# Optimization experiments

Hardware: AMD Instinct MI355X
Metric: run time of the kernel (lower is better)

The kernel has to match this reference:

```python
import jax, jax.numpy as jnp
import numpy as np

B, T, F = 1024, 256, 64
H1, H2, H3 = 64, 32, 16


def _lstm_params(key, in_dim, units, scale=0.1):
    k1, k2, k3 = jax.random.split(key, 3)
    W = jax.random.normal(k1, (in_dim, 4 * units), jnp.float32) * scale
    U = jax.random.normal(k2, (units, 4 * units), jnp.float32) * scale
    b = jax.random.normal(k3, (4 * units,), jnp.float32) * scale
    return W, U, b


def lstm_seq(x, W, U, b, reverse):
    """Keras-style LSTM (gate order i,f,g,o). Returns (all_h [B,T,H] time-aligned, last_h [B,H])."""
    Bx = x.shape[0]
    H = U.shape[0]
    xz = jnp.einsum('bti,ij->btj', x, W) + b  # [B,T,4H]
    if reverse:
        xz = xz[:, ::-1]
    xz = jnp.swapaxes(xz, 0, 1)  # [T,B,4H]

    def step(carry, zx):
        h, c = carry
        z = zx + h @ U
        i, f, g, o = jnp.split(z, 4, axis=-1)
        i = jax.nn.sigmoid(i)
        f = jax.nn.sigmoid(f)
        g = jnp.tanh(g)
        o = jax.nn.sigmoid(o)
        c = f * c + i * g
        h = o * jnp.tanh(c)
        return (h, c), h

    h0 = jnp.zeros((Bx, H), x.dtype)
    (hT, _), hs = jax.lax.scan(step, (h0, h0), xz)
    hs = jnp.swapaxes(hs, 0, 1)  # [B,T,H]
    if reverse:
        hs = hs[:, ::-1]  # Keras Bidirectional re-reverses backward outputs
    return hs, hT


def setup_inputs() -> dict:
    key = jax.random.key(0)
    ks = jax.random.split(key, 10)
    x = jax.random.normal(ks[0], (B, T, F), jnp.float32)
    W1f, U1f, b1f = _lstm_params(ks[1], F, H1)
    W1b, U1b, b1b = _lstm_params(ks[2], F, H1)
    W2f, U2f, b2f = _lstm_params(ks[3], 2 * H1, H2)
    W2b, U2b, b2b = _lstm_params(ks[4], 2 * H1, H2)
    W3f, U3f, b3f = _lstm_params(ks[5], 2 * H2, H3)
    W3b, U3b, b3b = _lstm_params(ks[6], 2 * H2, H3)
    Wd1 = jax.random.normal(ks[7], (2 * H3, 16), jnp.float32) * 0.1
    bd1 = jnp.zeros((16,), jnp.float32)
    Wd2 = jax.random.normal(ks[8], (16, 2), jnp.float32) * 0.1
    bd2 = jnp.zeros((2,), jnp.float32)
    return dict(inputs=x,
                W1f=W1f, U1f=U1f, b1f=b1f, W1b=W1b, U1b=U1b, b1b=b1b,
                W2f=W2f, U2f=U2f, b2f=b2f, W2b=W2b, U2b=U2b, b2b=b2b,
                W3f=W3f, U3f=U3f, b3f=b3f, W3b=W3b, U3b=U3b, b3b=b3b,
                Wd1=Wd1, bd1=bd1, Wd2=Wd2, bd2=bd2)


def reference(inputs,
              W1f, U1f, b1f, W1b, U1b, b1b,
              W2f, U2f, b2f, W2b, U2b, b2b,
              W3f, U3f, b3f, W3b, U3b, b3b,
              Wd1, bd1, Wd2, bd2):
    # inference path: all dropout / GaussianDropout layers are identity
    hf, _ = lstm_seq(inputs, W1f, U1f, b1f, reverse=False)
    hb, _ = lstm_seq(inputs, W1b, U1b, b1b, reverse=True)
    x = jnp.concatenate([hf, hb], axis=-1)  # [B,T,128]

    hf, _ = lstm_seq(x, W2f, U2f, b2f, reverse=False)
    hb, _ = lstm_seq(x, W2b, U2b, b2b, reverse=True)
    x = jnp.concatenate([hf, hb], axis=-1)  # [B,T,64]

    _, hf_last = lstm_seq(x, W3f, U3f, b3f, reverse=False)
    _, hb_last = lstm_seq(x, W3b, U3b, b3b, reverse=True)
    x = jnp.concatenate([hf_last, hb_last], axis=-1)  # [B,32] (Flatten is identity)

    x = jnp.clip(x @ Wd1 + bd1, 0.0, 6.0)  # relu6
    logits = x @ Wd2 + bd2
    return jax.nn.softmax(logits, axis=-1)
```

## Files before the change

kernel.cpp:

```cpp
#include <hip/hip_runtime.h>
#include <hip/hip_bf16.h>

#define T_SEQ 256
#define BATCH 1024

typedef __attribute__((ext_vector_type(8))) short  short8;
typedef __attribute__((ext_vector_type(4))) short  short4v;
typedef __attribute__((ext_vector_type(4))) float  floatx4;
typedef unsigned short ushort_t;
typedef unsigned int   uint_t;

template <int P> struct IC { static constexpr int v = P; };

constexpr float NL2E = -1.4426950408889634f;
constexpr float L2E2 =  2.8853900817779268f;

__device__ __forceinline__ float exp2_fast(float x) {
    float r; asm("v_exp_f32 %0, %1" : "=v"(r) : "v"(x)); return r;
}
__device__ __forceinline__ float rcp_fast(float x) {
    float r; asm("v_rcp_f32 %0, %1" : "=v"(r) : "v"(x)); return r;
}
__device__ __forceinline__ ushort_t f2bf(float f) {
    union { float f; uint_t u; } v; v.f = f;
    uint_t r = v.u + 0x7FFFu + ((v.u >> 16) & 1u);
    return (ushort_t)(r >> 16);
}
__device__ __forceinline__ uint_t pk_bf16(float a, float b) {
    union { __hip_bfloat162 h; uint_t u; } v;
    v.h = __float22bfloat162_rn(make_float2(a, b));
    return v.u;
}
__device__ __forceinline__ void sync_lds() {
    asm volatile("s_waitcnt lgkmcnt(0)\n\ts_barrier" ::: "memory");
}

__device__ __forceinline__ floatx4 mfma16(short4v a, short4v b, floatx4 c) {
#if __has_builtin(__builtin_amdgcn_mfma_f32_16x16x16bf16_1k)
    return __builtin_amdgcn_mfma_f32_16x16x16bf16_1k(a, b, c, 0, 0, 0);
#else
    floatx4 d;
    asm("v_mfma_f32_16x16x16_bf16 %0, %1, %2, %3" : "=v"(d) : "v"(a), "v"(b), "v"(c));
    return d;
#endif
}

template <int D, int H, bool IS_FIRST, bool SEQ_OUT, int MODE>
__global__ __launch_bounds__(MODE == 2 ? 64 : 64 * (H / 16), 1) void lstm_fused(
    const void* __restrict__ xin,
    const float* __restrict__ Wf, const float* __restrict__ Uf, const float* __restrict__ bgf,
    const float* __restrict__ Wb, const float* __restrict__ Ub, const float* __restrict__ bgb,
    void* __restrict__ outp)
{
    constexpr bool SW   = (MODE >= 1);
    constexpr bool REGH = (MODE == 2);
    constexpr int UG  = REGH ? 1 : H / 16;
    constexpr int NT  = REGH ? H / 16 : 1;
    constexpr int KSx = D / 32;
    constexpr int KSh = REGH ? 1 : (H + 31) / 32;
    constexpr int NC  = REGH ? H / 16 : 1;
    constexpr int HP  = (H < 32 ? 32 : H) + 8;
    constexpr int G4  = 4 * H;
    constexpr int NTH = 64 * UG;
    static_assert(D % 32 == 0 && T_SEQ % 4 == 0, "shape");

    const int tid  = threadIdx.x;
    const int ug   = tid >> 6;
    const int lane = tid & 63;
    const int lm   = lane & 15;
    const int lq   = lane >> 4;
    const int dir  = blockIdx.y;
    const int b0   = blockIdx.x * 16;

    const float* W  = dir ? Wb  : Wf;
    const float* U  = dir ? Ub  : Uf;
    const float* bg = dir ? bgb : bgf;

    __shared__ __align__(16) ushort_t hbuf[REGH ? 8 : 2 * 16 * HP];

    short8  aw[4][NT][KSx];
    short8  hw[4][NT][KSh];
    short4v uw[4][NT][NC];
    floatx4 bias4[4][NT];
#pragma unroll
    for (int g = 0; g < 4; g++) {
        const float sc = (g == 2) ? L2E2 : NL2E;
#pragma unroll
        for (int t = 0; t < NT; t++) {
            const int ub = g * H + (REGH ? t * 16 : ug * 16);
            floatx4 b4;
#pragma unroll
            for (int r = 0; r < 4; r++)
                b4[r] = sc * bg[ub + (SW ? lq * 4 + r : lm)];
            bias4[g][t] = b4;
            const int nc = ub + lm;
#pragma unroll
            for (int ks = 0; ks < KSx; ks++) {
                short8 f;
#pragma unroll
                for (int e = 0; e < 8; e++)
                    f[e] = (short)f2bf(sc * W[(ks * 32 + lq * 8 + e) * G4 + nc]);
                aw[g][t][ks] = f;
            }
            if constexpr (!REGH) {
#pragma unroll
                for (int ks = 0; ks < KSh; ks++) {
                    short8 f;
#pragma unroll
                    for (int e = 0; e < 8; e++) {
                        const int k = ks * 32 + lq * 8 + e;
                        f[e] = (k < H) ? (short)f2bf(sc * U[k * G4 + nc]) : (short)0;
                    }
                    hw[g][t][ks] = f;
                }
            } else {
#pragma unroll
                for (int c = 0; c < NC; c++) {
                    short4v f;
#pragma unroll
                    for (int e = 0; e < 4; e++)
                        f[e] = (short)f2bf(sc * U[(c * 16 + lq * 4 + e) * G4 + nc]);
                    uw[g][t][c] = f;
                }
            }
        }
    }

    if constexpr (!REGH) {
        for (int idx = tid; idx < 2 * 16 * HP; idx += NTH)
            hbuf[idx] = 0;
    }

    float   cst[NT][4];
    float   hl[NT][4];
    short4v hfrag[NC];
#pragma unroll
    for (int t = 0; t < NT; t++)
#pragma unroll
        for (int r = 0; r < 4; r++) { cst[t][r] = 0.f; hl[t][r] = 0.f; }
    if constexpr (REGH) {
#pragma unroll
        for (int c = 0; c < NC; c++) hfrag[c] = (short4v){0, 0, 0, 0};
    }

    const int t0 = dir ? T_SEQ - 1 : 0;
    const float*    pxf = (const float*)xin + ((size_t)(b0 + lm) * T_SEQ + t0) * D + lq * 8;
    const ushort_t* pxb = (const ushort_t*)xin + ((size_t)t0 * BATCH + b0 + lm) * D + lq * 8;
    const long xstepf = dir ? -(long)D : (long)D;
    const long xstepb = (dir ? -(long)BATCH : (long)BATCH) * D;
    ushort_t* pout;
    if constexpr (SW)
        pout = (ushort_t*)outp + ((size_t)t0 * BATCH + b0 + lm) * (2 * H) + dir * H +
               (REGH ? 0 : ug * 16) + lq * 4;
    else
        pout = (ushort_t*)outp + ((size_t)t0 * BATCH + b0 + lq * 4) * (2 * H) + dir * H +
               ug * 16 + lm;
    const long ostep = (dir ? -(long)BATCH : (long)BATCH) * (2 * H);

    float4 rawf[4][2 * KSx];
    short8 rawb[4][KSx];

    auto load_slot = [&](auto sl_) {
        constexpr int SL = decltype(sl_)::v;
        if (IS_FIRST) {
#pragma unroll
            for (int ks = 0; ks < KSx; ks++) {
                rawf[SL][2 * ks + 0] = *(const float4*)(pxf + ks * 32 + 0);
                rawf[SL][2 * ks + 1] = *(const float4*)(pxf + ks * 32 + 4);
            }
            pxf += xstepf;
        } else {
#pragma unroll
            for (int ks = 0; ks < KSx; ks++)
                rawb[SL][ks] = *(const short8*)(pxb + ks * 32);
            pxb += xstepb;
        }
    };

    load_slot(IC<0>{}); load_slot(IC<1>{}); load_slot(IC<2>{}); load_slot(IC<3>{});
    if constexpr (!REGH) __syncthreads();

    auto step = [&](auto p_, auto sl_, int s) {
        constexpr int P  = decltype(p_)::v;
        constexpr int SL = decltype(sl_)::v;

        short8 fh[KSh];
        if constexpr (!REGH) {
#pragma unroll
            for (int ks = 0; ks < KSh; ks++)
                fh[ks] = *(const short8*)&hbuf[(P * 16 + lm) * HP + ks * 32 + lq * 8];
        }

        short8 av[KSx];
        if (IS_FIRST) {
#pragma unroll
            for (int ks = 0; ks < KSx; ks++) {
                union { short8 s; uint_t u[4]; } f;
                const float* ra = (const float*)&rawf[SL][2 * ks];
#pragma unroll
                for (int e = 0; e < 4; e++) f.u[e] = pk_bf16(ra[2 * e], ra[2 * e + 1]);
                av[ks] = f.s;
            }
        } else {
#pragma unroll
            for (int ks = 0; ks < KSx; ks++) av[ks] = rawb[SL][ks];
        }

        floatx4 acc[4][NT];
#pragma unroll
        for (int g = 0; g < 4; g++)
#pragma unroll
            for (int t = 0; t < NT; t++)
                acc[g][t] = SW
                    ? __builtin_amdgcn_mfma_f32_16x16x32_bf16(aw[g][t][0], av[0], bias4[g][t], 0, 0, 0)
                    : __builtin_amdgcn_mfma_f32_16x16x32_bf16(av[0], aw[g][t][0], bias4[g][t], 0, 0, 0);
#pragma unroll
        for (int ks = 1; ks < KSx; ks++)
#pragma unroll
            for (int g = 0; g < 4; g++)
#pragma unroll
                for (int t = 0; t < NT; t++)
                    acc[g][t] = SW
                        ? __builtin_amdgcn_mfma_f32_16x16x32_bf16(aw[g][t][ks], av[ks], acc[g][t], 0, 0, 0)
                        : __builtin_amdgcn_mfma_f32_16x16x32_bf16(av[ks], aw[g][t][ks], acc[g][t], 0, 0, 0);

        if (s + 4 < T_SEQ) load_slot(sl_);

        if constexpr (!REGH) {
#pragma unroll
            for (int ks = 0; ks < KSh; ks++)
#pragma unroll
                for (int g = 0; g < 4; g++)
                    acc[g][0] = SW
                        ? __builtin_amdgcn_mfma_f32_16x16x32_bf16(hw[g][0][ks], fh[ks], acc[g][0], 0, 0, 0)
                        : __builtin_amdgcn_mfma_f32_16x16x32_bf16(fh[ks], hw[g][0][ks], acc[g][0], 0, 0, 0);
        } else {
#pragma unroll
            for (int c = 0; c < NC; c++)
#pragma unroll
                for (int g = 0; g < 4; g++)
#pragma unroll
                    for (int t = 0; t < NT; t++)
                        acc[g][t] = mfma16(uw[g][t][c], hfrag[c], acc[g][t]);
        }

#pragma unroll
        for (int t = 0; t < NT; t++) {
            float hv[4];
#pragma unroll
            for (int r = 0; r < 4; r++) {
                const float gi = rcp_fast(1.0f + exp2_fast(acc[0][t][r]));
                const float gf = rcp_fast(1.0f + exp2_fast(acc[1][t][r]));
                const float gg = 1.0f - 2.0f * rcp_fast(1.0f + exp2_fast(acc[2][t][r]));
                const float go = rcp_fast(1.0f + exp2_fast(acc[3][t][r]));
                cst[t][r] = fmaf(gf, cst[t][r], L2E2 * (gi * gg));
                const float tc = 1.0f - 2.0f * rcp_fast(1.0f + exp2_fast(cst[t][r]));
                hv[r] = go * tc;
            }
            if constexpr (SW) {
                const uint_t d0 = pk_bf16(hv[0], hv[1]);
                const uint_t d1 = pk_bf16(hv[2], hv[3]);
                if constexpr (REGH) {
                    union { uint_t u[2]; short4v s; } pp;
                    pp.u[0] = d0; pp.u[1] = d1;
                    hfrag[t] = pp.s;
                } else {
                    uint2 wv; wv.x = d0; wv.y = d1;
                    *(uint2*)&hbuf[((P ^ 1) * 16 + lm) * HP + ug * 16 + lq * 4] = wv;
                }
                if (SEQ_OUT) {
                    uint2 ov; ov.x = d0; ov.y = d1;
                    *(uint2*)&pout[t * 16] = ov;
                } else {
#pragma unroll
                    for (int r = 0; r < 4; r++) hl[t][r] = hv[r];
                }
            } else {
#pragma unroll
                for (int r = 0; r < 4; r++) {
                    const ushort_t hw_ = f2bf(hv[r]);
                    hbuf[((P ^ 1) * 16 + lq * 4 + r) * HP + ug * 16 + lm] = hw_;
                    if (SEQ_OUT) pout[r * 2 * H] = hw_;
                    else         hl[t][r] = hv[r];
                }
            }
        }
        pout += ostep;
        if (UG > 1) sync_lds();
    };

    for (int s = 0; s < T_SEQ; s += 4) {
        step(IC<0>{}, IC<0>{}, s);
        step(IC<1>{}, IC<1>{}, s + 1);
        step(IC<0>{}, IC<2>{}, s + 2);
        step(IC<1>{}, IC<3>{}, s + 3);
    }

    if (!SEQ_OUT) {
        float* op = (float*)outp;
        if constexpr (SW) {
#pragma unroll
            for (int t = 0; t < NT; t++) {
                float4 v4 = make_float4(hl[t][0], hl[t][1], hl[t][2], hl[t][3]);
                *(float4*)&op[(size_t)(b0 + lm) * (2 * H) + dir * H +
                              (REGH ? t * 16 : ug * 16) + lq * 4] = v4;
            }
        } else {
#pragma unroll
            for (int r = 0; r < 4; r++)
                op[(size_t)(b0 + lq * 4 + r) * (2 * H) + dir * H + ug * 16 + lm] = hl[0][r];
        }
    }
}

__global__ __launch_bounds__(256) void dense_head(
    const float* __restrict__ h3, const float* __restrict__ Wd1, const float* __restrict__ bd1,
    const float* __restrict__ Wd2, const float* __restrict__ bd2, float* __restrict__ out)
{
    const int b = blockIdx.x * blockDim.x + threadIdx.x;
    if (b >= BATCH) return;
    float x[32];
#pragma unroll
    for (int k = 0; k < 32; k++) x[k] = h3[b * 32 + k];
    float y[16];
#pragma unroll
    for (int jj = 0; jj < 16; jj++) {
        float a = bd1[jj];
#pragma unroll
        for (int k = 0; k < 32; k++) a = fmaf(x[k], Wd1[k * 16 + jj], a);
        y[jj] = fminf(fmaxf(a, 0.0f), 6.0f);
    }
    float l0 = bd2[0], l1 = bd2[1];
#pragma unroll
    for (int k = 0; k < 16; k++) {
        l0 = fmaf(y[k], Wd2[k * 2 + 0], l0);
        l1 = fmaf(y[k], Wd2[k * 2 + 1], l1);
    }
    const float m = fmaxf(l0, l1);
    const float e0 = __expf(l0 - m), e1 = __expf(l1 - m);
    const float inv = 1.0f / (e0 + e1);
    out[b * 2 + 0] = e0 * inv;
    out[b * 2 + 1] = e1 * inv;
}

extern "C" void kernel_launch(void* const* d_in, const int* in_sizes, int n_in,
                              void* d_out, int out_size, void* d_ws, size_t ws_size,
                              hipStream_t stream)
{
    const float* x   = (const float*)d_in[0];
    const float* W1f = (const float*)d_in[1];
    const float* U1f = (const float*)d_in[2];
    const float* b1f = (const float*)d_in[3];
    const float* W1b = (const float*)d_in[4];
    const float* U1b = (const float*)d_in[5];
    const float* b1b = (const float*)d_in[6];
    const float* W2f = (const float*)d_in[7];
    const float* U2f = (const float*)d_in[8];
    const float* b2f = (const float*)d_in[9];
    const float* W2b = (const float*)d_in[10];
    const float* U2b = (const float*)d_in[11];
    const float* b2b = (const float*)d_in[12];
    const float* W3f = (const float*)d_in[13];
    const float* U3f = (const float*)d_in[14];
    const float* b3f = (const float*)d_in[15];
    const float* W3b = (const float*)d_in[16];
    const float* U3b = (const float*)d_in[17];
    const float* b3b = (const float*)d_in[18];
    const float* Wd1 = (const float*)d_in[19];
    const float* bd1 = (const float*)d_in[20];
    const float* Wd2 = (const float*)d_in[21];
    const float* bd2 = (const float*)d_in[22];

    char* ws = (char*)d_ws;
    void*  l1out = (void*)ws;
    void*  l2out = (void*)(ws + (size_t)64 * 1024 * 1024);
    float* h3    = (float*)(ws + (size_t)96 * 1024 * 1024);
    float* out   = (float*)d_out;

    dim3 grid(BATCH / 16, 2);

    lstm_fused<64, 64, true, true, 0>
        <<<grid, 256, 0, stream>>>(x, W1f, U1f, b1f, W1b, U1b, b1b, l1out);
    lstm_fused<128, 32, false, true, 1>
        <<<grid, 128, 0, stream>>>(l1out, W2f, U2f, b2f, W2b, U2b, b2b, l2out);
    lstm_fused<64, 16, false, false, 1>
        <<<grid, 64, 0, stream>>>(l2out, W3f, U3f, b3f, W3b, U3b, b3b, h3);
    dense_head<<<dim3(BATCH / 256), 256, 0, stream>>>(h3, Wd1, bd1, Wd2, bd2, out);
}
```

Measured before the change: 506.0 us.

## Split recurrent MFMA chain and run both layer-3 directions in one wave

The recurrent h@U products in the fused LSTM kernel now go into separate zero-initialised accumulators, which are added to the input-projection accumulator before the gate activations. This lets the h-dependent MFMAs start without waiting on the x-projection chain, so the serial dependency per step is shorter. A new lstm_dual kernel handles forward and backward of layer 3 in one 64-thread block, interleaving the two independent recurrences to hide MFMA and transcendental latency. In exchange it halves the number of blocks for layer 3 and adds register pressure and extra vector adds per step.

```diff
diff --git a/kernel.cpp b/kernel.cpp
--- a/kernel.cpp
+++ b/kernel.cpp
@@ -62,7 +62,7 @@
     constexpr int HP  = (H < 32 ? 32 : H) + 8;
     constexpr int G4  = 4 * H;
     constexpr int NTH = 64 * UG;
-    static_assert(D % 32 == 0 && T_SEQ % 4 == 0, "shape");
+    static_assert(D % 32 == 0 && T_SEQ % 4 == 0 && KSh <= 2, "shape");
 
     const int tid  = threadIdx.x;
     const int ug   = tid >> 6;
@@ -131,6 +131,7 @@
             hbuf[idx] = 0;
     }
 
+    const floatx4 zero4 = {0.f, 0.f, 0.f, 0.f};
     float   cst[NT][4];
     float   hl[NT][4];
     short4v hfrag[NC];
@@ -206,12 +207,12 @@
             for (int ks = 0; ks < KSx; ks++) av[ks] = rawb[SL][ks];
         }
 
-        floatx4 acc[4][NT];
+        floatx4 accx[4][NT];
 #pragma unroll
         for (int g = 0; g < 4; g++)
 #pragma unroll
             for (int t = 0; t < NT; t++)
-                acc[g][t] = SW
+                accx[g][t] = SW
                     ? __builtin_amdgcn_mfma_f32_16x16x32_bf16(aw[g][t][0], av[0], bias4[g][t], 0, 0, 0)
                     : __builtin_amdgcn_mfma_f32_16x16x32_bf16(av[0], aw[g][t][0], bias4[g][t], 0, 0, 0);
 #pragma unroll
@@ -220,20 +221,31 @@
             for (int g = 0; g < 4; g++)
 #pragma unroll
                 for (int t = 0; t < NT; t++)
-                    acc[g][t] = SW
-                        ? __builtin_amdgcn_mfma_f32_16x16x32_bf16(aw[g][t][ks], av[ks], acc[g][t], 0, 0, 0)
-                        : __builtin_amdgcn_mfma_f32_16x16x32_bf16(av[ks], aw[g][t][ks], acc[g][t], 0, 0, 0);
+                    accx[g][t] = SW
+                        ? __builtin_amdgcn_mfma_f32_16x16x32_bf16(aw[g][t][ks], av[ks], accx[g][t], 0, 0, 0)
+                        : __builtin_amdgcn_mfma_f32_16x16x32_bf16(av[ks], aw[g][t][ks], accx[g][t], 0, 0, 0);
 
         if (s + 4 < T_SEQ) load_slot(sl_);
 
+        floatx4 acch[4][NT];
+        floatx4 acch2[4][NT];
         if constexpr (!REGH) {
 #pragma unroll
-            for (int ks = 0; ks < KSh; ks++)
+            for (int g = 0; g < 4; g++)
+#pragma unroll
+                for (int t = 0; t < NT; t++)
+                    acch[g][t] = SW
+                        ? __builtin_amdgcn_mfma_f32_16x16x32_bf16(hw[g][t][0], fh[0], zero4, 0, 0, 0)
+                        : __builtin_amdgcn_mfma_f32_16x16x32_bf16(fh[0], hw[g][t][0], zero4, 0, 0, 0);
+            if constexpr (KSh == 2) {
 #pragma unroll
                 for (int g = 0; g < 4; g++)
-                    acc[g][0] = SW
-                        ? __builtin_amdgcn_mfma_f32_16x16x32_bf16(hw[g][0][ks], fh[ks], acc[g][0], 0, 0, 0)
-                        : __builtin_amdgcn_mfma_f32_16x16x32_bf16(fh[ks], hw[g][0][ks], acc[g][0], 0, 0, 0);
+#pragma unroll
+                    for (int t = 0; t < NT; t++)
+                        acch2[g][t] = SW
+                            ? __builtin_amdgcn_mfma_f32_16x16x32_bf16(hw[g][t][1], fh[1], zero4, 0, 0, 0)
+                            : __builtin_amdgcn_mfma_f32_16x16x32_bf16(fh[1], hw[g][t][1], zero4, 0, 0, 0);
+            }
         } else {
 #pragma unroll
             for (int c = 0; c < NC; c++)
@@ -241,18 +253,25 @@
                 for (int g = 0; g < 4; g++)
 #pragma unroll
                     for (int t = 0; t < NT; t++)
-                        acc[g][t] = mfma16(uw[g][t][c], hfrag[c], acc[g][t]);
+                        accx[g][t] = mfma16(uw[g][t][c], hfrag[c], accx[g][t]);
         }
 
 #pragma unroll
         for (int t = 0; t < NT; t++) {
+            floatx4 zf[4];
+#pragma unroll
+            for (int g = 0; g < 4; g++) {
+                if constexpr (REGH)          zf[g] = accx[g][t];
+                else if constexpr (KSh == 2) zf[g] = accx[g][t] + acch[g][t] + acch2[g][t];
+                else                         zf[g] = accx[g][t] + acch[g][t];
+            }
             float hv[4];
 #pragma unroll
             for (int r = 0; r < 4; r++) {
-                const float gi = rcp_fast(1.0f + exp2_fast(acc[0][t][r]));
-                const float gf = rcp_fast(1.0f + exp2_fast(acc[1][t][r]));
-                const float gg = 1.0f - 2.0f * rcp_fast(1.0f + exp2_fast(acc[2][t][r]));
-                const float go = rcp_fast(1.0f + exp2_fast(acc[3][t][r]));
+                const float gi = rcp_fast(1.0f + exp2_fast(zf[0][r]));
+                const float gf = rcp_fast(1.0f + exp2_fast(zf[1][r]));
+                const float gg = 1.0f - 2.0f * rcp_fast(1.0f + exp2_fast(zf[2][r]));
+                const float go = rcp_fast(1.0f + exp2_fast(zf[3][r]));
                 cst[t][r] = fmaf(gf, cst[t][r], L2E2 * (gi * gg));
                 const float tc = 1.0f - 2.0f * rcp_fast(1.0f + exp2_fast(cst[t][r]));
                 hv[r] = go * tc;
@@ -310,6 +329,145 @@
             for (int r = 0; r < 4; r++)
                 op[(size_t)(b0 + lq * 4 + r) * (2 * H) + dir * H + ug * 16 + lm] = hl[0][r];
         }
+    }
+}
+
+template <int D, int H>
+__global__ __launch_bounds__(64, 1) void lstm_dual(
+    const void* __restrict__ xin,
+    const float* __restrict__ Wf, const float* __restrict__ Uf, const float* __restrict__ bgf,
+    const float* __restrict__ Wb, const float* __restrict__ Ub, const float* __restrict__ bgb,
+    float* __restrict__ outp)
+{
+    constexpr int KSx = D / 32;
+    constexpr int HP  = (H < 32 ? 32 : H) + 8;
+    constexpr int G4  = 4 * H;
+    static_assert(D % 32 == 0 && H <= 32 && T_SEQ % 2 == 0, "dual shape");
+
+    const int lane = threadIdx.x & 63;
+    const int lm   = lane & 15;
+    const int lq   = lane >> 4;
+    const int b0   = blockIdx.x * 16;
+
+    __shared__ __align__(16) ushort_t hbuf[2][2][16][HP];
+
+    short8  aw[2][4][KSx];
+    short8  hw[2][4];
+    floatx4 bias4[2][4];
+#pragma unroll
+    for (int dd = 0; dd < 2; dd++) {
+        const float* W  = dd ? Wb  : Wf;
+        const float* U  = dd ? Ub  : Uf;
+        const float* bg = dd ? bgb : bgf;
+#pragma unroll
+        for (int g = 0; g < 4; g++) {
+            const float sc = (g == 2) ? L2E2 : NL2E;
+            floatx4 b4;
+#pragma unroll
+            for (int r = 0; r < 4; r++) b4[r] = sc * bg[g * H + lq * 4 + r];
+            bias4[dd][g] = b4;
+            const int nc = g * H + lm;
+#pragma unroll
+            for (int ks = 0; ks < KSx; ks++) {
+                short8 f;
+#pragma unroll
+                for (int e = 0; e < 8; e++)
+                    f[e] = (short)f2bf(sc * W[(ks * 32 + lq * 8 + e) * G4 + nc]);
+                aw[dd][g][ks] = f;
+            }
+            short8 f;
+#pragma unroll
+            for (int e = 0; e < 8; e++) {
+                const int k = lq * 8 + e;
+                f[e] = (k < H) ? (short)f2bf(sc * U[k * G4 + nc]) : (short)0;
+            }
+            hw[dd][g] = f;
+        }
+    }
+    for (int idx = lane; idx < 2 * 2 * 16 * HP; idx += 64)
+        ((ushort_t*)hbuf)[idx] = 0;
+
+    float cst[2][4], hl[2][4];
+#pragma unroll
+    for (int dd = 0; dd < 2; dd++)
+#pragma unroll
+        for (int r = 0; r < 4; r++) { cst[dd][r] = 0.f; hl[dd][r] = 0.f; }
+
+    const ushort_t* px0 = (const ushort_t*)xin + ((size_t)b0 + lm) * D + lq * 8;
+    const ushort_t* px1 = (const ushort_t*)xin +
+        ((size_t)(T_SEQ - 1) * BATCH + b0 + lm) * D + lq * 8;
+    const long xst = (long)BATCH * D;
+
+    short8 ring[2][2][KSx];
+    auto load2 = [&](auto sl_) {
+        constexpr int SL = decltype(sl_)::v;
+#pragma unroll
+        for (int ks = 0; ks < KSx; ks++) ring[0][SL][ks] = *(const short8*)(px0 + ks * 32);
+        px0 += xst;
+#pragma unroll
+        for (int ks = 0; ks < KSx; ks++) ring[1][SL][ks] = *(const short8*)(px1 + ks * 32);
+        px1 -= xst;
+    };
+    load2(IC<0>{}); load2(IC<1>{});
+
+    auto stepd = [&](auto p_, int s) {
+        constexpr int P = decltype(p_)::v;
+        short8 fh0 = *(const short8*)&hbuf[0][P][lm][lq * 8];
+        short8 fh1 = *(const short8*)&hbuf[1][P][lm][lq * 8];
+
+        floatx4 acc[2][4];
+#pragma unroll
+        for (int dd = 0; dd < 2; dd++)
+#pragma unroll
+            for (int g = 0; g < 4; g++)
+                acc[dd][g] = __builtin_amdgcn_mfma_f32_16x16x32_bf16(
+                    aw[dd][g][0], ring[dd][P][0], bias4[dd][g], 0, 0, 0);
+#pragma unroll
+        for (int ks = 1; ks < KSx; ks++)
+#pragma unroll
+            for (int dd = 0; dd < 2; dd++)
+#pragma unroll
+                for (int g = 0; g < 4; g++)
+                    acc[dd][g] = __builtin_amdgcn_mfma_f32_16x16x32_bf16(
+                        aw[dd][g][ks], ring[dd][P][ks], acc[dd][g], 0, 0, 0);
+
+        if (s + 2 < T_SEQ) load2(p_);
+
+#pragma unroll
+        for (int g = 0; g < 4; g++)
+            acc[0][g] = __builtin_amdgcn_mfma_f32_16x16x32_bf16(hw[0][g], fh0, acc[0][g], 0, 0, 0);
+#pragma unroll
+        for (int g = 0; g < 4; g++)
+            acc[1][g] = __builtin_amdgcn_mfma_f32_16x16x32_bf16(hw[1][g], fh1, acc[1][g], 0, 0, 0);
+
+#pragma unroll
+        for (int dd = 0; dd < 2; dd++) {
+            float hv[4];
+#pragma unroll
+            for (int r = 0; r < 4; r++) {
+                const float gi = rcp_fast(1.0f + exp2_fast(acc[dd][0][r]));
+                const float gf = rcp_fast(1.0f + exp2_fast(acc[dd][1][r]));
+                const float gg = 1.0f - 2.0f * rcp_fast(1.0f + exp2_fast(acc[dd][2][r]));
+                const float go = rcp_fast(1.0f + exp2_fast(acc[dd][3][r]));
+                cst[dd][r] = fmaf(gf, cst[dd][r], L2E2 * (gi * gg));
+                const float tc = 1.0f - 2.0f * rcp_fast(1.0f + exp2_fast(cst[dd][r]));
+                hv[r] = go * tc;
+                hl[dd][r] = hv[r];
+            }
+            uint2 wv; wv.x = pk_bf16(hv[0], hv[1]); wv.y = pk_bf16(hv[2], hv[3]);
+            *(uint2*)&hbuf[dd][P ^ 1][lm][lq * 4] = wv;
+        }
+    };
+
+    for (int s = 0; s < T_SEQ; s += 2) {
+        stepd(IC<0>{}, s);
+        stepd(IC<1>{}, s + 1);
+    }
+
+#pragma unroll
+    for (int dd = 0; dd < 2; dd++) {
+        float4 v4 = make_float4(hl[dd][0], hl[dd][1], hl[dd][2], hl[dd][3]);
+        *(float4*)&outp[(size_t)(b0 + lm) * (2 * H) + dd * H + lq * 4] = v4;
     }
 }
 
@@ -383,7 +541,7 @@
         <<<grid, 256, 0, stream>>>(x, W1f, U1f, b1f, W1b, U1b, b1b, l1out);
     lstm_fused<128, 32, false, true, 1>
         <<<grid, 128, 0, stream>>>(l1out, W2f, U2f, b2f, W2b, U2b, b2b, l2out);
-    lstm_fused<64, 16, false, false, 1>
-        <<<grid, 64, 0, stream>>>(l2out, W3f, U3f, b3f, W3b, U3b, b3b, h3);
+    lstm_dual<64, 16>
+        <<<dim3(BATCH / 16), 64, 0, stream>>>(l2out, W3f, U3f, b3f, W3b, U3b, b3b, h3);
     dense_head<<<dim3(BATCH / 256), 256, 0, stream>>>(h3, Wd1, bd1, Wd2, bd2, out);
 }
```

Result: slower. 626.1 us (+23.7%).

## Split layer-3 LSTM into parallel input GEMM and lightweight recurrent kernel

Applied to the files above, without the earlier changes.

Replaces the fused layer-3 LSTM kernel with two kernels. The first is a fully parallel MFMA GEMM that precomputes the scaled input projections for both directions and stores them as fp16. The second is a recurrence kernel that streams those precomputed gate inputs with a 4-deep register prefetch and does only the small h@U MFMA per step. This takes the input projection off the serial critical path. In exchange it adds an extra workspace round trip of fp16 activations and slightly lower input-projection precision.

```diff
diff --git a/kernel.cpp b/kernel.cpp
--- a/kernel.cpp
+++ b/kernel.cpp
@@ -1,5 +1,6 @@
 #include <hip/hip_runtime.h>
 #include <hip/hip_bf16.h>
+#include <hip/hip_fp16.h>
 
 #define T_SEQ 256
 #define BATCH 1024
@@ -30,6 +31,14 @@
     union { __hip_bfloat162 h; uint_t u; } v;
     v.h = __float22bfloat162_rn(make_float2(a, b));
     return v.u;
+}
+__device__ __forceinline__ uint_t pk_f16(float a, float b) {
+    const uint_t lo = (uint_t)__half_as_ushort(__float2half_rn(a));
+    const uint_t hi = (uint_t)__half_as_ushort(__float2half_rn(b));
+    return lo | (hi << 16);
+}
+__device__ __forceinline__ float h2f(uint_t u) {
+    return __half2float(__ushort_as_half((ushort_t)u));
 }
 __device__ __forceinline__ void sync_lds() {
     asm volatile("s_waitcnt lgkmcnt(0)\n\ts_barrier" ::: "memory");
@@ -311,6 +320,149 @@
                 op[(size_t)(b0 + lq * 4 + r) * (2 * H) + dir * H + ug * 16 + lm] = hl[0][r];
         }
     }
+}
+
+__global__ __launch_bounds__(256) void xz_gemm(
+    const ushort_t* __restrict__ xin,
+    const float* __restrict__ Wf, const float* __restrict__ bgf,
+    const float* __restrict__ Wb, const float* __restrict__ bgb,
+    ushort_t* __restrict__ xz)
+{
+    constexpr int DIN = 64, HH = 16, G4 = 64, KS = 2;
+    const int tid = threadIdx.x, ug = tid >> 6, lane = tid & 63;
+    const int lm = lane & 15, lq = lane >> 4;
+
+    short8  aw[2][4][KS];
+    floatx4 bias4[2][4];
+#pragma unroll
+    for (int dd = 0; dd < 2; dd++) {
+        const float* W  = dd ? Wb  : Wf;
+        const float* bg = dd ? bgb : bgf;
+#pragma unroll
+        for (int g = 0; g < 4; g++) {
+            const float sc = (g == 2) ? L2E2 : NL2E;
+            floatx4 b4;
+#pragma unroll
+            for (int r = 0; r < 4; r++) b4[r] = sc * bg[g * HH + lq * 4 + r];
+            bias4[dd][g] = b4;
+#pragma unroll
+            for (int ks = 0; ks < KS; ks++) {
+                short8 f;
+#pragma unroll
+                for (int e = 0; e < 8; e++)
+                    f[e] = (short)f2bf(sc * W[(ks * 32 + lq * 8 + e) * G4 + g * HH + lm]);
+                aw[dd][g][ks] = f;
+            }
+        }
+    }
+
+    const int NW    = gridDim.x * 4;
+    const int w0    = blockIdx.x * 4 + ug;
+    const int NTILE = (T_SEQ * BATCH) / 16;
+    for (int tile = w0; tile < NTILE; tile += NW) {
+        const size_t row = (size_t)tile * 16 + lm;
+        short8 xv[KS];
+#pragma unroll
+        for (int ks = 0; ks < KS; ks++)
+            xv[ks] = *(const short8*)&xin[row * DIN + ks * 32 + lq * 8];
+#pragma unroll
+        for (int dd = 0; dd < 2; dd++)
+#pragma unroll
+            for (int g = 0; g < 4; g++) {
+                floatx4 a = __builtin_amdgcn_mfma_f32_16x16x32_bf16(aw[dd][g][0], xv[0], bias4[dd][g], 0, 0, 0);
+                a = __builtin_amdgcn_mfma_f32_16x16x32_bf16(aw[dd][g][1], xv[1], a, 0, 0, 0);
+                uint2 st;
+                st.x = pk_f16(a[0], a[1]);
+                st.y = pk_f16(a[2], a[3]);
+                *(uint2*)&xz[row * 128 + dd * 64 + g * HH + lq * 4] = st;
+            }
+    }
+}
+
+template <int H>
+__global__ __launch_bounds__(64, 1) void lstm_rec(
+    const ushort_t* __restrict__ xz,
+    const float* __restrict__ Uf, const float* __restrict__ Ub,
+    float* __restrict__ outp)
+{
+    static_assert(H == 16 && T_SEQ % 4 == 0, "rec shape");
+    const int lane = threadIdx.x & 63;
+    const int lm   = lane & 15;
+    const int lq   = lane >> 4;
+    const int dir  = blockIdx.y;
+    const int b0   = blockIdx.x * 16;
+    const float* U = dir ? Ub : Uf;
+
+    short4v uw[4];
+#pragma unroll
+    for (int g = 0; g < 4; g++) {
+        const float sc = (g == 2) ? L2E2 : NL2E;
+        short4v f;
+#pragma unroll
+        for (int e = 0; e < 4; e++)
+            f[e] = (short)f2bf(sc * U[(lq * 4 + e) * (4 * H) + g * H + lm]);
+        uw[g] = f;
+    }
+
+    short4v hfrag = (short4v){0, 0, 0, 0};
+    float cst[4] = {0.f, 0.f, 0.f, 0.f};
+    float hl[4]  = {0.f, 0.f, 0.f, 0.f};
+
+    const int t0 = dir ? T_SEQ - 1 : 0;
+    const ushort_t* pz = xz + ((size_t)t0 * BATCH + b0 + lm) * 128 + dir * 64 + lq * 4;
+    const long zstep = (dir ? -(long)BATCH : (long)BATCH) * 128;
+
+    uint2 rz[4][4];
+    auto load_slot = [&](auto sl_) {
+        constexpr int SL = decltype(sl_)::v;
+#pragma unroll
+        for (int g = 0; g < 4; g++)
+            rz[SL][g] = *(const uint2*)(pz + g * 16);
+        pz += zstep;
+    };
+    load_slot(IC<0>{}); load_slot(IC<1>{}); load_slot(IC<2>{}); load_slot(IC<3>{});
+
+    auto step = [&](auto sl_, int s) {
+        constexpr int SL = decltype(sl_)::v;
+        floatx4 acc[4];
+#pragma unroll
+        for (int g = 0; g < 4; g++) {
+            floatx4 zc;
+            zc[0] = h2f(rz[SL][g].x & 0xffffu);
+            zc[1] = h2f(rz[SL][g].x >> 16);
+            zc[2] = h2f(rz[SL][g].y & 0xffffu);
+            zc[3] = h2f(rz[SL][g].y >> 16);
+            acc[g] = mfma16(uw[g], hfrag, zc);
+        }
+        if (s + 4 < T_SEQ) load_slot(sl_);
+
+        float hv[4];
+#pragma unroll
+        for (int r = 0; r < 4; r++) {
+            const float gi = rcp_fast(1.0f + exp2_fast(acc[0][r]));
+            const float gf = rcp_fast(1.0f + exp2_fast(acc[1][r]));
+            const float gg = 1.0f - 2.0f * rcp_fast(1.0f + exp2_fast(acc[2][r]));
+            const float go = rcp_fast(1.0f + exp2_fast(acc[3][r]));
+            cst[r] = fmaf(gf, cst[r], L2E2 * (gi * gg));
+            const float tc = 1.0f - 2.0f * rcp_fast(1.0f + exp2_fast(cst[r]));
+            hv[r] = go * tc;
+            hl[r] = hv[r];
+        }
+        union { uint_t u[2]; short4v s4; } pp;
+        pp.u[0] = pk_bf16(hv[0], hv[1]);
+        pp.u[1] = pk_bf16(hv[2], hv[3]);
+        hfrag = pp.s4;
+    };
+
+    for (int s = 0; s < T_SEQ; s += 4) {
+        step(IC<0>{}, s);
+        step(IC<1>{}, s + 1);
+        step(IC<2>{}, s + 2);
+        step(IC<3>{}, s + 3);
+    }
+
+    float4 v4 = make_float4(hl[0], hl[1], hl[2], hl[3]);
+    *(float4*)&outp[(size_t)(b0 + lm) * (2 * H) + dir * H + lq * 4] = v4;
 }
 
 __global__ __launch_bounds__(256) void dense_head(
@@ -372,10 +524,11 @@
     const float* bd2 = (const float*)d_in[22];
 
     char* ws = (char*)d_ws;
-    void*  l1out = (void*)ws;
-    void*  l2out = (void*)(ws + (size_t)64 * 1024 * 1024);
-    float* h3    = (float*)(ws + (size_t)96 * 1024 * 1024);
-    float* out   = (float*)d_out;
+    void*     l1out = (void*)ws;
+    void*     l2out = (void*)(ws + (size_t)64 * 1024 * 1024);
+    ushort_t* xz3   = (ushort_t*)ws;
+    float*    h3    = (float*)(ws + (size_t)96 * 1024 * 1024);
+    float*    out   = (float*)d_out;
 
     dim3 grid(BATCH / 16, 2);
 
@@ -383,7 +536,9 @@
         <<<grid, 256, 0, stream>>>(x, W1f, U1f, b1f, W1b, U1b, b1b, l1out);
     lstm_fused<128, 32, false, true, 1>
         <<<grid, 128, 0, stream>>>(l1out, W2f, U2f, b2f, W2b, U2b, b2b, l2out);
-    lstm_fused<64, 16, false, false, 1>
-        <<<grid, 64, 0, stream>>>(l2out, W3f, U3f, b3f, W3b, U3b, b3b, h3);
+    xz_gemm
+        <<<dim3(256), 256, 0, stream>>>((const ushort_t*)l2out, W3f, b3f, W3b, b3b, xz3);
+    lstm_rec<16>
+        <<<grid, 64, 0, stream>>>(xz3, U3f, U3b, h3);
     dense_head<<<dim3(BATCH / 256), 256, 0, stream>>>(h3, Wd1, bd1, Wd2, bd2, out);
 }
```

Result: slower. 518.2 us (+2.4%).
